# Optimization experiments

Measured on AMD Instinct MI355X. Metric: run time of the kernel, lower is better.

The kernel has to match this reference:

```python
import jax, jax.numpy as jnp
import numpy as np
from jax import lax

D_MODEL = 512
D_STATE = 32
D_CONV = 4
D_INNER = 2 * D_MODEL
DT_RANK = (D_MODEL + 15) // 16  # 32
B_SZ, L = 8, 1024
EPS = 1e-12


def _mamba_params(key, pfx):
    ks = jax.random.split(key, 6)
    s = 0.02
    p = {}
    p[pfx + '_in_w'] = jax.random.normal(ks[0], (2 * D_INNER, D_MODEL)) * s
    p[pfx + '_conv_w'] = jax.random.normal(ks[1], (D_INNER, D_CONV)) * s
    p[pfx + '_conv_b'] = jnp.zeros((D_INNER,))
    p[pfx + '_xproj_w'] = jax.random.normal(ks[2], (DT_RANK + 2 * D_STATE, D_INNER)) * s
    p[pfx + '_dt_w'] = jax.random.normal(ks[3], (D_INNER, DT_RANK)) * s
    p[pfx + '_dt_b'] = jax.random.uniform(ks[4], (D_INNER,), minval=-4.0, maxval=-2.0)
    p[pfx + '_A_log'] = jnp.log(jnp.broadcast_to(jnp.arange(1, D_STATE + 1, dtype=jnp.float32), (D_INNER, D_STATE)))
    p[pfx + '_D'] = jnp.ones((D_INNER,))
    p[pfx + '_out_w'] = jax.random.normal(ks[5], (D_MODEL, D_INNER)) * s
    return p


def setup_inputs() -> dict:
    key = jax.random.key(0)
    ks = jax.random.split(key, 10)
    inp = {
        'hidden_states': jax.random.normal(ks[0], (B_SZ, L, D_MODEL)),
        'lengths': jax.random.randint(ks[1], (B_SZ,), 1, L + 1, dtype=jnp.int32),
    }
    inp.update(_mamba_params(ks[2], 'f'))
    inp.update(_mamba_params(ks[3], 'b'))
    s = 0.02
    inp['proj_w'] = jax.random.normal(ks[4], (1, 2)) * 0.5 + 0.5
    inp['proj_b'] = jnp.zeros((1,))
    inp['ln_g'] = jnp.ones((D_MODEL,))
    inp['ln_b'] = jnp.zeros((D_MODEL,))
    inp['ffn_w1'] = jax.random.normal(ks[5], (4 * D_MODEL, D_MODEL)) * s
    inp['ffn_b1'] = jnp.zeros((4 * D_MODEL,))
    inp['ffn_w2'] = jax.random.normal(ks[6], (D_MODEL, 4 * D_MODEL)) * s
    inp['ffn_b2'] = jnp.zeros((D_MODEL,))
    inp['ffn_ln_g'] = jnp.ones((D_MODEL,))
    inp['ffn_ln_b'] = jnp.zeros((D_MODEL,))
    return inp


def _layernorm(x, g, b):
    mu = jnp.mean(x, -1, keepdims=True)
    var = jnp.mean(jnp.square(x - mu), -1, keepdims=True)
    return (x - mu) * lax.rsqrt(var + EPS) * g + b


def _selective_scan(delta, Bm, Cm, u, A, D):
    # delta,u: (B,L,Di); Bm,Cm: (B,L,N); A: (Di,N); D: (Di,)
    def step(h, inp):
        d_t, B_t, C_t, u_t = inp
        dA = jnp.exp(d_t[..., None] * A)                 # (B,Di,N)
        h = dA * h + (d_t * u_t)[..., None] * B_t[:, None, :]
        y = jnp.einsum('bdn,bn->bd', h, C_t)
        return h, y
    h0 = jnp.zeros((u.shape[0], A.shape[0], A.shape[1]), u.dtype)
    xs = (delta.transpose(1, 0, 2), Bm.transpose(1, 0, 2),
          Cm.transpose(1, 0, 2), u.transpose(1, 0, 2))
    _, ys = lax.scan(step, h0, xs)
    return ys.transpose(1, 0, 2) + u * D


def _mamba(x, in_w, conv_w, conv_b, xproj_w, dt_w, dt_b, A_log, Dp, out_w):
    xz = jnp.einsum('bld,ed->ble', x, in_w)              # (B,L,2Di)
    x_in, z = jnp.split(xz, 2, axis=-1)
    # causal depthwise conv1d
    xc = jnp.pad(x_in.transpose(0, 2, 1), ((0, 0), (0, 0), (D_CONV - 1, 0)))
    xc = lax.conv_general_dilated(xc, conv_w[:, None, :], (1,), 'VALID',
                                  dimension_numbers=('NCH', 'OIH', 'NCH'),
                                  feature_group_count=D_INNER)
    xc = jax.nn.silu(xc + conv_b[None, :, None]).transpose(0, 2, 1)  # (B,L,Di)
    x_dbl = jnp.einsum('bld,ed->ble', xc, xproj_w)
    dt, Bm, Cm = jnp.split(x_dbl, [DT_RANK, DT_RANK + D_STATE], axis=-1)
    delta = jax.nn.softplus(jnp.einsum('blr,dr->bld', dt, dt_w) + dt_b)
    A = -jnp.exp(A_log)
    y = _selective_scan(delta, Bm, Cm, xc, A, Dp)
    y = y * jax.nn.silu(z)
    return jnp.einsum('bld,ed->ble', y, out_w)


def reference(hidden_states, lengths,
              f_in_w, f_conv_w, f_conv_b, f_xproj_w, f_dt_w, f_dt_b, f_A_log, f_D, f_out_w,
              b_in_w, b_conv_w, b_conv_b, b_xproj_w, b_dt_w, b_dt_b, b_A_log, b_D, b_out_w,
              proj_w, proj_b, ln_g, ln_b,
              ffn_w1, ffn_b1, ffn_w2, ffn_b2, ffn_ln_g, ffn_ln_b):
    x = hidden_states
    hf = _mamba(x, f_in_w, f_conv_w, f_conv_b, f_xproj_w, f_dt_w, f_dt_b, f_A_log, f_D, f_out_w)
    hb = _mamba(jnp.flip(x, 1), b_in_w, b_conv_w, b_conv_b, b_xproj_w, b_dt_w, b_dt_b, b_A_log, b_D, b_out_w)
    hb = jnp.flip(hb, 1)
    # Linear(2,1) over stacked [hf,hb] on last axis
    out = hf * proj_w[0, 0] + hb * proj_w[0, 1] + proj_b[0]
    out1 = _layernorm(out + x, ln_g, ln_b)  # dropout = identity (eval)
    h = jax.nn.gelu(jnp.einsum('bld,ed->ble', out1, ffn_w1) + ffn_b1, approximate=False)
    h = jnp.einsum('ble,de->bld', h, ffn_w2) + ffn_b2
    return _layernorm(h + out1, ffn_ln_g, ffn_ln_b)
```

## Files before the change

### kernel.cpp

```cpp
#include <hip/hip_runtime.h>
#include <hip/hip_bf16.h>
#include <hip/hip_fp16.h>
#include <math.h>

typedef __hip_bfloat16 bf16;
typedef __attribute__((ext_vector_type(8))) short bfrag;
typedef __attribute__((ext_vector_type(4))) float ffrag;
typedef __attribute__((ext_vector_type(4))) float f4;
typedef __attribute__((ext_vector_type(4))) short sh4;

#define BSZ    8
#define LSEQ   1024
#define DMODEL 512
#define DINNER 1024
#define DSTATE 32
#define DTRANK 32
#define MROWS  (BSZ * LSEQ)

__device__ __forceinline__ float bf2f(bf16 v) { return __bfloat162float(v); }
__device__ __forceinline__ float s2f(short s) {
    union { unsigned u; float f; } c; c.u = ((unsigned)(unsigned short)s) << 16; return c.f;
}
__device__ __forceinline__ short f2s(float v) {
    union { bf16 b; short s; } u; u.b = __float2bfloat16(v); return u.s;
}
__device__ __forceinline__ void stC(float* p, size_t i, float v) { p[i] = v; }
__device__ __forceinline__ void stC(bf16* p, size_t i, float v) { p[i] = __float2bfloat16(v); }
__device__ __forceinline__ float fsigmoid(float x) {
    return __builtin_amdgcn_rcpf(1.f + __expf(-x));
}
__device__ __forceinline__ float fexp2(float x) { return __builtin_amdgcn_exp2f(x); }

__device__ __forceinline__ float dload(const void* p, size_t i, int f) {
    if (f == 1) return ((const float*)p)[i];
    if (f == 2) return __half2float(((const __half*)p)[i]);
    if (f == 3) return (float)((const double*)p)[i];
    return bf2f(((const bf16*)p)[i]);
}

enum { ACT_NONE = 0, ACT_SOFTPLUS = 1, ACT_GELU = 2 };

__global__ void resolve_kernel(const void* a8, const void* d9, const void* d22,
                               const void* s0, const void* s1, int* flags)
{
    if (blockIdx.x != 0) return;
    const int lane = threadIdx.x;
    const int cand[4] = {1, 0, 2, 3};
    int fw = -1;
    for (int ci = 0; ci < 4 && fw < 0; ++ci) {
        int f = cand[ci];
        bool ok = true;
        if (lane < 48) {
            float e = logf((float)((lane & 31) + 1));
            float v = dload(a8, lane, f);
            ok = (v == v) && fabsf(v - e) <= 0.02f * e + 0.02f;
        } else if (lane < 56) {
            int k = lane - 48;
            ok = fabsf(dload(d9, k, f) - 1.f) <= 0.01f &&
                 fabsf(dload(d22, k, f) - 1.f) <= 0.01f;
        }
        if (__all(ok)) fw = f;
    }
    int fx = -1, xs = -1;
    for (int si = 0; si < 2 && fx < 0; ++si) {
        const void* p = (si == 0) ? s0 : s1;
        for (int ci = 0; ci < 4 && fx < 0; ++ci) {
            int f = cand[ci];
            bool ok = true;
            float s = 0.f, s2 = 0.f;
            for (int k = lane; k < 256; k += 64) {
                float v = dload(p, k, f);
                ok = ok && (v == v) && fabsf(v) < 16.f;
                s += v; s2 += v * v;
            }
            int allok = __all(ok);
            for (int m = 1; m < 64; m <<= 1) {
                s += __shfl_xor(s, m); s2 += __shfl_xor(s2, m);
            }
            if (allok) {
                float mu = s * (1.f / 256.f);
                float var = s2 * (1.f / 256.f) - mu * mu;
                if (var > 0.25f && var < 4.f) { fx = f; xs = si; }
            }
        }
    }
    if (lane == 0) {
        flags[0] = (fw < 0) ? 1 : fw;
        flags[1] = (fx < 0) ? 1 : fx;
        flags[2] = (xs < 0) ? 0 : xs;
        flags[3] = (fw == 1 && fx == 1) ? 1 : 0;
    }
}

__global__ __launch_bounds__(256) void cvt_x_kernel(const void* x0, const void* x1,
                                                    bf16* __restrict__ dst,
                                                    const int* __restrict__ flags)
{
    const void* x = flags[2] ? x1 : x0;
    const int fx = flags[1];
    int i = blockIdx.x * 256 + threadIdx.x;
    if (fx == 1) {
        f4 v = ((const f4*)x)[i];
        sh4 o;
#pragma unroll
        for (int j = 0; j < 4; ++j) o[j] = f2s(v[j]);
        ((sh4*)dst)[i] = o;
    } else {
#pragma unroll
        for (int j = 0; j < 4; ++j)
            dst[(size_t)i * 4 + j] = __float2bfloat16(dload(x, (size_t)i * 4 + j, fx));
    }
}

__device__ __forceinline__ void cvt_one(const float* s, bf16* d, int off)
{
    f4 v = ((const f4*)s)[off];
    sh4 o;
#pragma unroll
    for (int j = 0; j < 4; ++j) o[j] = f2s(v[j]);
    ((sh4*)d)[off] = o;
}

__global__ __launch_bounds__(256) void cvt6_kernel(
    const float* s0, bf16* d0, int n0, const float* s1, bf16* d1, int n1,
    const float* s2, bf16* d2, int n2, const float* s3, bf16* d3, int n3,
    const float* s4, bf16* d4, int n4, const float* s5, bf16* d5, int n5)
{
    int i = blockIdx.x * 256 + threadIdx.x;
    if (i < n0) { cvt_one(s0, d0, i); return; } i -= n0;
    if (i < n1) { cvt_one(s1, d1, i); return; } i -= n1;
    if (i < n2) { cvt_one(s2, d2, i); return; } i -= n2;
    if (i < n3) { cvt_one(s3, d3, i); return; } i -= n3;
    if (i < n4) { cvt_one(s4, d4, i); return; } i -= n4;
    if (i < n5) cvt_one(s5, d5, i);
}

__global__ __launch_bounds__(256) void transpose_kernel(
    const bf16* __restrict__ src, bf16* __restrict__ dst, int R, int D)
{
    __shared__ short t[64][72];
    const int r0 = blockIdx.x * 64, d0 = blockIdx.y * 64;
    const int tr = threadIdx.x >> 3;
    const int tc = (threadIdx.x & 7) * 8;
#pragma unroll
    for (int h = 0; h < 2; ++h) {
        int d = tr + h * 32;
        bfrag v = *(const bfrag*)&src[(size_t)(d0 + d) * R + r0 + tc];
#pragma unroll
        for (int j = 0; j < 8; ++j) t[tc + j][d] = v[j];
    }
    __syncthreads();
#pragma unroll
    for (int h = 0; h < 2; ++h) {
        int r = tr + h * 32;
        bfrag v = *(const bfrag*)&t[r][tc];
        *(bfrag*)&dst[(size_t)(r0 + r) * D + d0 + tc] = v;
    }
}

__global__ __launch_bounds__(256) void conv8_kernel(
    const bf16* __restrict__ xin_T,
    const void* __restrict__ cw, const void* __restrict__ cb,
    bf16* __restrict__ u_T,
    const int* __restrict__ flags)
{
    const int fw = flags[0];
    int blk = blockIdx.x;
    int chunk = blk & 3;
    int d = blk >> 2;
    int m = chunk * 2048 + threadIdx.x * 8;
    size_t base = (size_t)d * MROWS;
    float w0 = dload(cw, d * 4 + 0, fw), w1 = dload(cw, d * 4 + 1, fw);
    float w2 = dload(cw, d * 4 + 2, fw), w3 = dload(cw, d * 4 + 3, fw);
    float cbv = dload(cb, d, fw);
    const bf16* src = &xin_T[base + m];
    bfrag v = *(const bfrag*)src;
    float x[11];
    if (m & (LSEQ - 1)) {
        bfrag pv = *(const bfrag*)(src - 8);
        x[0] = s2f(pv[5]); x[1] = s2f(pv[6]); x[2] = s2f(pv[7]);
    } else { x[0] = 0.f; x[1] = 0.f; x[2] = 0.f; }
#pragma unroll
    for (int j = 0; j < 8; ++j) x[3 + j] = s2f(v[j]);
    bfrag o;
#pragma unroll
    for (int j = 0; j < 8; ++j) {
        float a = cbv + x[j] * w0 + x[j + 1] * w1 + x[j + 2] * w2 + x[j + 3] * w3;
        a = a * fsigmoid(a);
        o[j] = f2s(a);
    }
    *(bfrag*)&u_T[base + m] = o;
}

__device__ __forceinline__ void glds16(const bf16* g, short* l)
{
    __builtin_amdgcn_global_load_lds(
        (const __attribute__((address_space(1))) void*)g,
        (__attribute__((address_space(3))) void*)l,
        16, 0, 0);
}

template <int FLIPB, int ACT, typename CT>
__global__ __launch_bounds__(256) void bgemm_kernel(
    const bf16* __restrict__ A, int lda,
    const bf16* __restrict__ B, int ldb,
    const float* __restrict__ bias,
    CT* __restrict__ C, int ldc, int K)
{
    __shared__ __align__(16) short As[2][128 * 32];
    __shared__ __align__(16) short Bs[2][128 * 32];
    const int tid = threadIdx.x;
    const int bm = blockIdx.y * 128, bn = blockIdx.x * 128;
    const int lane = tid & 63, w = tid >> 6;

    const int srow = lane >> 2;
    const int skc  = (lane & 3) << 3;
    const int arow0 = bm + w * 32 + srow;
    int brow0 = bn + w * 32 + srow;
    int brow1 = brow0 + 16;
    if (FLIPB) {
        brow0 = (brow0 & ~(LSEQ - 1)) + (LSEQ - 1 - (brow0 & (LSEQ - 1)));
        brow1 = (brow1 & ~(LSEQ - 1)) + (LSEQ - 1 - (brow1 & (LSEQ - 1)));
    }
    const bf16* ga0 = A + (size_t)arow0 * lda + skc;
    const bf16* ga1 = ga0 + (size_t)16 * lda;
    const bf16* gb0 = B + (size_t)brow0 * ldb + skc;
    const bf16* gb1 = B + (size_t)brow1 * ldb + skc;
    const int lA0 = (w * 32) * 32, lA1 = (w * 32 + 16) * 32;

    const int wm = (w & 1) << 6, wn = (w >> 1) << 6;
    const int lm = lane & 15, quad = lane >> 4;

    ffrag acc[4][4];
#pragma unroll
    for (int i = 0; i < 4; ++i)
#pragma unroll
        for (int j = 0; j < 4; ++j)
#pragma unroll
            for (int e = 0; e < 4; ++e) acc[i][j][e] = 0.f;

#define BG_STAGE(buf, kk)                      \
    do {                                       \
        glds16(ga0 + (kk), &As[buf][lA0]);     \
        glds16(ga1 + (kk), &As[buf][lA1]);     \
        glds16(gb0 + (kk), &Bs[buf][lA0]);     \
        glds16(gb1 + (kk), &Bs[buf][lA1]);     \
    } while (0)

#define BG_COMPUTE(buf)                                                        \
    do {                                                                       \
        bfrag af[4], bfv[4];                                                   \
        _Pragma("unroll")                                                      \
        for (int ti = 0; ti < 4; ++ti)                                         \
            af[ti] = *(const bfrag*)&As[buf][(wm + ti * 16 + lm) * 32 + quad * 8]; \
        _Pragma("unroll")                                                      \
        for (int tj = 0; tj < 4; ++tj)                                         \
            bfv[tj] = *(const bfrag*)&Bs[buf][(wn + tj * 16 + lm) * 32 + quad * 8]; \
        __builtin_amdgcn_s_setprio(1);                                         \
        _Pragma("unroll")                                                      \
        for (int ti = 0; ti < 4; ++ti)                                         \
            _Pragma("unroll")                                                  \
            for (int tj = 0; tj < 4; ++tj)                                     \
                acc[ti][tj] = __builtin_amdgcn_mfma_f32_16x16x32_bf16(         \
                    af[ti], bfv[tj], acc[ti][tj], 0, 0, 0);                    \
        __builtin_amdgcn_s_setprio(0);                                         \
    } while (0)

    BG_STAGE(0, 0);
    BG_STAGE(1, 32);
    int cur = 0;
    for (int k0 = 0; k0 < K - 32; k0 += 32) {
        asm volatile("s_waitcnt vmcnt(4)" ::: "memory");
        __builtin_amdgcn_s_barrier();
        __builtin_amdgcn_sched_barrier(0);
        BG_COMPUTE(cur);
        __builtin_amdgcn_s_barrier();
        __builtin_amdgcn_sched_barrier(0);
        if (k0 + 64 < K) BG_STAGE(cur, k0 + 64);
        cur ^= 1;
    }
    asm volatile("s_waitcnt vmcnt(0)" ::: "memory");
    __builtin_amdgcn_s_barrier();
    __builtin_amdgcn_sched_barrier(0);
    BG_COMPUTE(cur);
#undef BG_STAGE
#undef BG_COMPUTE

#pragma unroll
    for (int tj = 0; tj < 4; ++tj) {
        int col = bn + wn + tj * 16 + lm;
        float bcv = bias ? bias[col] : 0.f;
#pragma unroll
        for (int ti = 0; ti < 4; ++ti) {
#pragma unroll
            for (int r2 = 0; r2 < 4; ++r2) {
                int rowg = bm + wm + ti * 16 + quad * 4 + r2;
                float v = acc[ti][tj][r2] + bcv;
                if (ACT == ACT_GELU) v = 0.5f * v * (1.f + erff(v * 0.70710678118654752f));
                stC(C, (size_t)rowg * ldc + col, v);
            }
        }
    }
}

template <int ACT, int XPROJ, int RES, typename CT>
__global__ __launch_bounds__(256) void bgemm64_kernel(
    const bf16* __restrict__ A, int lda,
    const bf16* __restrict__ B, int ldb,
    const float* __restrict__ bias,
    CT* __restrict__ C, int ldc,
    float* __restrict__ C2,
    const bf16* __restrict__ res,
    int M, int K)
{
    __shared__ __align__(16) short As[2][128 * 64];
    __shared__ __align__(16) short Bs[2][64 * 64];
    const int tid = threadIdx.x;
    const int bm = blockIdx.y * 128, bn = blockIdx.x * 64;
    const int lane = tid & 63, w = tid >> 6;

    const int lr = lane >> 3;
    const int sc = ((lane & 7) ^ lr) << 3;

    const bf16* ga[4];
#pragma unroll
    for (int a = 0; a < 4; ++a) {
        int ar = bm + w * 32 + a * 8 + lr;
        if (ar >= M) ar = M - 1;
        ga[a] = A + (size_t)ar * lda + sc;
    }
    const bf16* gb[2];
#pragma unroll
    for (int a = 0; a < 2; ++a) {
        int br = bn + w * 16 + a * 8 + lr;
        gb[a] = B + (size_t)br * ldb + sc;
    }
    const int lA = (w * 32) * 64, lB = (w * 16) * 64;

    const int wm = (w & 1) << 6, wn = (w >> 1) << 5;
    const int lm = lane & 15, quad = lane >> 4;

    ffrag acc[4][2];
#pragma unroll
    for (int i = 0; i < 4; ++i)
#pragma unroll
        for (int j = 0; j < 2; ++j)
#pragma unroll
            for (int e = 0; e < 4; ++e) acc[i][j][e] = 0.f;

#define BG64_STAGE(buf, kk)                                              \
    do {                                                                 \
        _Pragma("unroll")                                                \
        for (int a = 0; a < 4; ++a)                                      \
            glds16(ga[a] + (kk), &As[buf][lA + a * 8 * 64]);             \
        _Pragma("unroll")                                                \
        for (int a = 0; a < 2; ++a)                                      \
            glds16(gb[a] + (kk), &Bs[buf][lB + a * 8 * 64]);             \
    } while (0)

#define BG64_COMPUTE(buf)                                                      \
    do {                                                                       \
        bfrag af[2][4], bfv[2][2];                                             \
        _Pragma("unroll")                                                      \
        for (int kk = 0; kk < 2; ++kk) {                                       \
            _Pragma("unroll")                                                  \
            for (int ti = 0; ti < 4; ++ti) {                                   \
                int row = wm + ti * 16 + lm;                                   \
                int c = kk * 4 + quad;                                         \
                af[kk][ti] = *(const bfrag*)&As[buf][row * 64 + ((c ^ (row & 7)) << 3)]; \
            }                                                                  \
            _Pragma("unroll")                                                  \
            for (int tj = 0; tj < 2; ++tj) {                                   \
                int row = wn + tj * 16 + lm;                                   \
                int c = kk * 4 + quad;                                         \
                bfv[kk][tj] = *(const bfrag*)&Bs[buf][row * 64 + ((c ^ (row & 7)) << 3)]; \
            }                                                                  \
        }                                                                      \
        __builtin_amdgcn_s_setprio(1);                                         \
        _Pragma("unroll")                                                      \
        for (int kk = 0; kk < 2; ++kk)                                         \
            _Pragma("unroll")                                                  \
            for (int ti = 0; ti < 4; ++ti)                                     \
                _Pragma("unroll")                                              \
                for (int tj = 0; tj < 2; ++tj)                                 \
                    acc[ti][tj] = __builtin_amdgcn_mfma_f32_16x16x32_bf16(     \
                        af[kk][ti], bfv[kk][tj], acc[ti][tj], 0, 0, 0);        \
        __builtin_amdgcn_s_setprio(0);                                         \
    } while (0)

    BG64_STAGE(0, 0);
    BG64_STAGE(1, 64);
    int cur = 0;
    for (int k0 = 0; k0 < K - 64; k0 += 64) {
        asm volatile("s_waitcnt vmcnt(6)" ::: "memory");
        __builtin_amdgcn_s_barrier();
        __builtin_amdgcn_sched_barrier(0);
        BG64_COMPUTE(cur);
        __builtin_amdgcn_s_barrier();
        __builtin_amdgcn_sched_barrier(0);
        if (k0 + 128 < K) BG64_STAGE(cur, k0 + 128);
        cur ^= 1;
    }
    asm volatile("s_waitcnt vmcnt(0)" ::: "memory");
    __builtin_amdgcn_s_barrier();
    __builtin_amdgcn_sched_barrier(0);
    BG64_COMPUTE(cur);
#undef BG64_STAGE
#undef BG64_COMPUTE

#pragma unroll
    for (int tj = 0; tj < 2; ++tj) {
        int col = bn + wn + tj * 16 + lm;
        float bcv = bias ? bias[col] : 0.f;
#pragma unroll
        for (int ti = 0; ti < 4; ++ti) {
#pragma unroll
            for (int r2 = 0; r2 < 4; ++r2) {
                int rowg = bm + wm + ti * 16 + quad * 4 + r2;
                if (XPROJ) {
                    float v = acc[ti][tj][r2];
                    if (rowg < 32)
                        ((float*)C)[(size_t)rowg * ldc + col] = v;
                    else if (rowg < 96)
                        C2[(((size_t)col >> 3) * 64 + (rowg - 32)) * 8 + (col & 7)] = v;
                } else if (rowg < M) {
                    float v = acc[ti][tj][r2] + bcv;
                    if (ACT == ACT_GELU) v = 0.5f * v * (1.f + erff(v * 0.70710678118654752f));
                    if (RES) v += bf2f(res[(size_t)rowg * ldc + col]);
                    stC(C, (size_t)rowg * ldc + col, v);
                }
            }
        }
    }
}

__global__ __launch_bounds__(256) void dt_kernel(
    const float* __restrict__ xdT,
    const float* __restrict__ dt_w,
    const float* __restrict__ dt_b,
    bf16* __restrict__ delta_T)
{
    const int m = blockIdx.x * 256 + threadIdx.x;
    const int d0 = blockIdx.y * 64;
    float v[32];
#pragma unroll
    for (int r = 0; r < 32; ++r) v[r] = xdT[(size_t)r * MROWS + m];
    for (int d = d0; d < d0 + 64; ++d) {
        float acc = dt_b[d];
#pragma unroll
        for (int r = 0; r < 32; ++r) acc = fmaf(dt_w[d * 32 + r], v[r], acc);
        acc = (acc > 20.f) ? acc : log1pf(__expf(acc));
        delta_T[(size_t)d * MROWS + m] = __float2bfloat16(acc);
    }
}

#define SCH 8
struct ScanBuf { float dl[SCH], uv[SCH], Bv[SCH], Cv[SCH]; float zsc, usc; };

__device__ __forceinline__ void scan_load(ScanBuf& s,
    const bf16* __restrict__ dT, const bf16* __restrict__ uT,
    const bf16* __restrict__ zT, const float* __restrict__ xm,
    size_t lb, int coff, int n)
{
    bfrag dv = *(const bfrag*)&dT[lb];
    bfrag uv = *(const bfrag*)&uT[lb];
#pragma unroll
    for (int j = 0; j < SCH; ++j) { s.dl[j] = s2f(dv[j]); s.uv[j] = s2f(uv[j]); }
    s.zsc = bf2f(zT[lb + (n & 7)]);
    s.usc = bf2f(uT[lb + (n & 7)]);
    const float* bp = xm + coff + n * 8;
    f4 b0 = *(const f4*)bp;
    f4 b1 = *(const f4*)(bp + 4);
    const float* cp = bp + 256;
    f4 c0 = *(const f4*)cp;
    f4 c1 = *(const f4*)(cp + 4);
#pragma unroll
    for (int j = 0; j < 4; ++j) {
        s.Bv[j] = b0[j]; s.Bv[4 + j] = b1[j];
        s.Cv[j] = c0[j]; s.Cv[4 + j] = c1[j];
    }
}

__device__ __forceinline__ void scan_compute(const ScanBuf& s, float& h,
    float Ad2, float Dd, bf16* __restrict__ yT, size_t lb,
    bool b0, bool b1, bool b2, bool wr)
{
    float p[SCH];
#pragma unroll
    for (int j = 0; j < SCH; ++j) {
        float dlv = s.dl[j];
        h = fexp2(dlv * Ad2) * h + dlv * s.uv[j] * s.Bv[j];
        p[j] = h * s.Cv[j];
    }
    float q[4];
#pragma unroll
    for (int jj = 0; jj < 4; ++jj) {
        float keep = b0 ? p[2 * jj + 1] : p[2 * jj];
        float send = b0 ? p[2 * jj] : p[2 * jj + 1];
        q[jj] = keep + __shfl_xor(send, 1);
    }
    float r0 = (b1 ? q[1] : q[0]) + __shfl_xor(b1 ? q[0] : q[1], 2);
    float r1 = (b1 ? q[3] : q[2]) + __shfl_xor(b1 ? q[2] : q[3], 2);
    float t = (b2 ? r1 : r0) + __shfl_xor(b2 ? r0 : r1, 4);
    t += __shfl_xor(t, 8);
    t += __shfl_xor(t, 16);
    if (wr) {
        float y = t + s.usc * Dd;
        float g = s.zsc;
        y *= g * fsigmoid(g);
        yT[lb + (threadIdx.x & 7)] = __float2bfloat16(y);
    }
}

__global__ __launch_bounds__(256) void scan_kernel(
    const bf16* __restrict__ delta_T,
    bf16* __restrict__ u_T,
    const bf16* __restrict__ z_T,
    const float* __restrict__ xdbl_m,
    const void* __restrict__ A_log,
    const void* __restrict__ Dp,
    const int* __restrict__ flags)
{
    const int fw = flags[0];
    const int tid = threadIdx.x;
    const int n = tid & 31;
    const int dloc = tid >> 5;
    const int gd = blockIdx.x * 8 + dloc;
    const int b = gd >> 10;
    const int d = gd & (DINNER - 1);
    const bool b0 = n & 1, b1 = n & 2, b2 = n & 4;
    const bool wr = (n < 8);

    const float Ad2 = -__expf(dload(A_log, d * DSTATE + n, fw)) * 1.44269504088896341f;
    const float Dd = dload(Dp, d, fw);
    const size_t lbase = (size_t)d * MROWS + b * LSEQ;
    const float* xmb = xdbl_m + ((size_t)b * LSEQ >> 3) * 512;
    float h = 0.f;

    ScanBuf bufA, bufB;
    scan_load(bufA, delta_T, u_T, z_T, xmb, lbase, 0, n);
    for (int c0 = 0; c0 < LSEQ / SCH; c0 += 2) {
        scan_load(bufB, delta_T, u_T, z_T, xmb,
                  lbase + (size_t)(c0 + 1) * SCH, (c0 + 1) * 512, n);
        scan_compute(bufA, h, Ad2, Dd, u_T, lbase + (size_t)c0 * SCH, b0, b1, b2, wr);
        if (c0 + 2 < LSEQ / SCH)
            scan_load(bufA, delta_T, u_T, z_T, xmb,
                      lbase + (size_t)(c0 + 2) * SCH, (c0 + 2) * 512, n);
        scan_compute(bufB, h, Ad2, Dd, u_T, lbase + (size_t)(c0 + 1) * SCH, b0, b1, b2, wr);
    }
}

__global__ __launch_bounds__(256) void combine_cvt_kernel(
    const bf16* __restrict__ hf, const bf16* __restrict__ hb,
    const void* __restrict__ x0, const void* __restrict__ x1,
    const void* __restrict__ pw, const void* __restrict__ pb,
    const void* __restrict__ g, const void* __restrict__ be,
    bf16* __restrict__ out1,
    const float* __restrict__ w1s, bf16* __restrict__ w1d,
    const float* __restrict__ w2s, bf16* __restrict__ w2d,
    const int* __restrict__ flags)
{
    if (blockIdx.x >= 2048) {
        int i = (blockIdx.x - 2048) * 256 + threadIdx.x;
        const int nw = (2048 * 512) / 4;
        if (i < nw) cvt_one(w1s, w1d, i);
        else cvt_one(w2s, w2d, i - nw);
        return;
    }
    const int fw = flags[0];
    const int fx = flags[1];
    const void* x = flags[2] ? x1 : x0;
    const int lane = threadIdx.x & 63;
    int row = blockIdx.x * 4 + (threadIdx.x >> 6);
    int b = row >> 10, l = row & (LSEQ - 1);
    int rrow = (b << 10) + (LSEQ - 1 - l);
    float pw0 = dload(pw, 0, fw), pw1 = dload(pw, 1, fw), pbv = dload(pb, 0, fw);
    int c0 = lane * 8;
    bfrag hfv = *(const bfrag*)&hf[(size_t)row * DMODEL + c0];
    bfrag hbv = *(const bfrag*)&hb[(size_t)rrow * DMODEL + c0];
    float v[8], s = 0.f, s2 = 0.f;
#pragma unroll
    for (int j = 0; j < 8; ++j) {
        float val = s2f(hfv[j]) * pw0 + s2f(hbv[j]) * pw1 + pbv
                  + dload(x, (size_t)row * DMODEL + c0 + j, fx);
        v[j] = val; s += val; s2 += val * val;
    }
#pragma unroll
    for (int m = 1; m < 64; m <<= 1) { s += __shfl_xor(s, m); s2 += __shfl_xor(s2, m); }
    float mu = s * (1.f / DMODEL);
    float var = s2 * (1.f / DMODEL) - mu * mu;
    float r = rsqrtf(fmaxf(var, 0.f) + 1e-12f);
    bfrag o;
#pragma unroll
    for (int j = 0; j < 8; ++j)
        o[j] = f2s((v[j] - mu) * r * dload(g, c0 + j, fw) + dload(be, c0 + j, fw));
    *(bfrag*)&out1[(size_t)row * DMODEL + c0] = o;
}

__global__ __launch_bounds__(256) void final_ln_kernel(
    const float* __restrict__ out2,
    const void* __restrict__ g, const void* __restrict__ be,
    float* __restrict__ out,
    const int* __restrict__ flags)
{
    const int fw = flags[0];
    const int valid = flags[3];
    const int lane = threadIdx.x & 63;
    int row = blockIdx.x * 4 + (threadIdx.x >> 6);
    int c0 = lane * 8;
    f4 a0 = *(const f4*)&out2[(size_t)row * DMODEL + c0];
    f4 a1 = *(const f4*)&out2[(size_t)row * DMODEL + c0 + 4];
    float v[8], s = 0.f, s2 = 0.f;
#pragma unroll
    for (int j = 0; j < 4; ++j) { v[j] = a0[j]; v[4 + j] = a1[j]; }
#pragma unroll
    for (int j = 0; j < 8; ++j) { s += v[j]; s2 += v[j] * v[j]; }
#pragma unroll
    for (int m = 1; m < 64; m <<= 1) { s += __shfl_xor(s, m); s2 += __shfl_xor(s2, m); }
    float mu = s * (1.f / DMODEL);
    float var = s2 * (1.f / DMODEL) - mu * mu;
    float r = rsqrtf(fmaxf(var, 0.f) + 1e-12f);
    f4 o0, o1;
#pragma unroll
    for (int j = 0; j < 8; ++j) {
        float val = (v[j] - mu) * r * dload(g, c0 + j, fw) + dload(be, c0 + j, fw);
        val = valid ? val : 0.f;
        if (j < 4) o0[j] = val; else o1[j - 4] = val;
    }
    *(f4*)&out[(size_t)row * DMODEL + c0] = o0;
    *(f4*)&out[(size_t)row * DMODEL + c0 + 4] = o1;
}

extern "C" void kernel_launch(void* const* d_in, const int* in_sizes, int n_in,
                              void* d_out, int out_size, void* d_ws, size_t ws_size,
                              hipStream_t stream)
{
    const void* x0 = d_in[0];
    const void* x1 = d_in[1];
    const void* proj_w   = d_in[20];
    const void* proj_b   = d_in[21];
    const void* ln_g     = d_in[22];
    const void* ln_b     = d_in[23];
    const float* ffn_w1  = (const float*)d_in[24];
    const float* ffn_b1  = (const float*)d_in[25];
    const float* ffn_w2  = (const float*)d_in[26];
    const float* ffn_b2  = (const float*)d_in[27];
    const void* ffn_ln_g = d_in[28];
    const void* ffn_ln_b = d_in[29];

    char* wsb = (char*)d_ws;
    char* ob  = (char*)d_out;
    bf16*  xin_T   = (bf16*)(wsb + 0);
    bf16*  z_T     = (bf16*)(wsb + (16u << 20));
    bf16*  uy_T    = (bf16*)(wsb + (32u << 20));
    bf16*  u_rm    = (bf16*)(wsb + 0);
    bf16*  delta_T = (bf16*)(wsb + 0);
    bf16*  y_rm    = (bf16*)(wsb + 0);
    float* xdT     = (float*)(wsb + (48u << 20));
    bf16*  in_w_bf0 = (bf16*)(wsb + (49u << 20));
    float* xdbl_m   = (float*)(wsb + (49u << 20));
    bf16*  in_w_bf1 = (bf16*)(wsb + (51u << 20));
    bf16*  xp_w_bf0 = (bf16*)(wsb + (53u << 20));
    bf16*  xp_w_bf1 = (bf16*)(wsb + (53u << 20) + (256u << 10));
    bf16*  o_w_bf0  = (bf16*)(wsb + (54u << 20));
    bf16*  o_w_bf1  = (bf16*)(wsb + (55u << 20));
    bf16*  hf      = (bf16*)d_out;
    bf16*  hb      = (bf16*)d_out + (size_t)MROWS * DMODEL;
    bf16*  xbf     = (bf16*)(ob + (8u << 20));
    bf16*  w1bf    = (bf16*)(ob + 0);
    bf16*  w2bf    = (bf16*)(ob + (2u << 20));
    bf16*  out1    = (bf16*)(wsb + 0);
    bf16*  ffn_h   = (bf16*)(wsb + (8u << 20));
    float* out2    = (float*)(wsb + (40u << 20));
    int*   flags   = (int*)(wsb + (56u << 20));

    dim3 blk(256);

    resolve_kernel<<<dim3(1), dim3(64), 0, stream>>>(
        d_in[8], d_in[9], d_in[22], x0, x1, flags);
    cvt_x_kernel<<<dim3(4096), blk, 0, stream>>>(x0, x1, xbf, flags);
    cvt6_kernel<<<dim3(3264), blk, 0, stream>>>(
        (const float*)d_in[2],  in_w_bf0, (2048 * 512) / 4,
        (const float*)d_in[11], in_w_bf1, (2048 * 512) / 4,
        (const float*)d_in[5],  xp_w_bf0, (96 * 1024) / 4,
        (const float*)d_in[14], xp_w_bf1, (96 * 1024) / 4,
        (const float*)d_in[10], o_w_bf0,  (512 * 1024) / 4,
        (const float*)d_in[19], o_w_bf1,  (512 * 1024) / 4);

    for (int dir = 0; dir < 2; ++dir) {
        int pb0 = 2 + dir * 9;
        const void*  conv_w  = d_in[pb0 + 1];
        const void*  conv_b  = d_in[pb0 + 2];
        const float* dt_w    = (const float*)d_in[pb0 + 4];
        const float* dt_b    = (const float*)d_in[pb0 + 5];
        const void*  A_log   = d_in[pb0 + 6];
        const void*  Dp      = d_in[pb0 + 7];
        bf16* in_w_bf = dir ? in_w_bf1 : in_w_bf0;
        bf16* xp_w_bf = dir ? xp_w_bf1 : xp_w_bf0;
        bf16* o_w_bf  = dir ? o_w_bf1  : o_w_bf0;
        bf16* hout = (dir == 0) ? hf : hb;

        if (dir == 0)
            bgemm_kernel<0, ACT_NONE, bf16><<<dim3(64, 16), blk, 0, stream>>>(
                in_w_bf, DMODEL, xbf, DMODEL, nullptr, xin_T, MROWS, DMODEL);
        else
            bgemm_kernel<1, ACT_NONE, bf16><<<dim3(64, 16), blk, 0, stream>>>(
                in_w_bf, DMODEL, xbf, DMODEL, nullptr, xin_T, MROWS, DMODEL);

        conv8_kernel<<<dim3(DINNER * 4), blk, 0, stream>>>(
            xin_T, conv_w, conv_b, uy_T, flags);
        transpose_kernel<<<dim3(128, 16), blk, 0, stream>>>(uy_T, u_rm, MROWS, DINNER);
        bgemm64_kernel<ACT_NONE, 1, 0, float><<<dim3(128, 1), blk, 0, stream>>>(
            xp_w_bf, DINNER, u_rm, DINNER, nullptr,
            xdT, MROWS, xdbl_m, nullptr, 96, DINNER);
        dt_kernel<<<dim3(32, 16), blk, 0, stream>>>(xdT, dt_w, dt_b, delta_T);
        scan_kernel<<<dim3((BSZ * DINNER) / 8), blk, 0, stream>>>(
            delta_T, uy_T, z_T, xdbl_m, A_log, Dp, flags);
        transpose_kernel<<<dim3(128, 16), blk, 0, stream>>>(uy_T, y_rm, MROWS, DINNER);
        bgemm64_kernel<ACT_NONE, 0, 0, bf16><<<dim3(8, 64), blk, 0, stream>>>(
            y_rm, DINNER, o_w_bf, DINNER, nullptr, hout, DMODEL, nullptr, nullptr,
            MROWS, DINNER);
    }

    combine_cvt_kernel<<<dim3(4096), blk, 0, stream>>>(
        hf, hb, x0, x1, proj_w, proj_b, ln_g, ln_b, out1,
        ffn_w1, w1bf, ffn_w2, w2bf, flags);
    bgemm_kernel<0, ACT_GELU, bf16><<<dim3(16, 64), blk, 0, stream>>>(
        out1, DMODEL, w1bf, DMODEL, ffn_b1, ffn_h, 2048, DMODEL);
    bgemm64_kernel<ACT_NONE, 0, 1, float><<<dim3(8, 64), blk, 0, stream>>>(
        ffn_h, 2048, w2bf, 2048, ffn_b2, out2, DMODEL, nullptr, out1,
        MROWS, 2048);
    final_ln_kernel<<<dim3(MROWS / 4), blk, 0, stream>>>(
        out2, ffn_ln_g, ffn_ln_b, (float*)d_out, flags);
}
```

Baseline: 807.4 us.

## Triple-buffer GEMM LDS pipeline and fuse dtype resolve into weight conversion

The bf16 GEMM goes from a double-buffered to a triple-buffered LDS pipeline that prefetches two K-steps ahead, with vmcnt waits graded by how many stages remain. The goal is to hide more global-load latency behind MFMA work. The cost is 50% more shared memory per block, which may lower occupancy. Separately, the one-block dtype-resolve kernel is merged into the weight-conversion kernel as an extra block, removing one launch.

```diff
diff --git a/kernel.cpp b/kernel.cpp
--- a/kernel.cpp
+++ b/kernel.cpp
@@ -40,56 +40,79 @@
 
 enum { ACT_NONE = 0, ACT_SOFTPLUS = 1, ACT_GELU = 2 };
 
-__global__ void resolve_kernel(const void* a8, const void* d9, const void* d22,
-                               const void* s0, const void* s1, int* flags)
-{
-    if (blockIdx.x != 0) return;
-    const int lane = threadIdx.x;
-    const int cand[4] = {1, 0, 2, 3};
-    int fw = -1;
-    for (int ci = 0; ci < 4 && fw < 0; ++ci) {
-        int f = cand[ci];
-        bool ok = true;
-        if (lane < 48) {
-            float e = logf((float)((lane & 31) + 1));
-            float v = dload(a8, lane, f);
-            ok = (v == v) && fabsf(v - e) <= 0.02f * e + 0.02f;
-        } else if (lane < 56) {
-            int k = lane - 48;
-            ok = fabsf(dload(d9, k, f) - 1.f) <= 0.01f &&
-                 fabsf(dload(d22, k, f) - 1.f) <= 0.01f;
-        }
-        if (__all(ok)) fw = f;
-    }
-    int fx = -1, xs = -1;
-    for (int si = 0; si < 2 && fx < 0; ++si) {
-        const void* p = (si == 0) ? s0 : s1;
-        for (int ci = 0; ci < 4 && fx < 0; ++ci) {
+__device__ __forceinline__ void cvt_one(const float* s, bf16* d, int off)
+{
+    f4 v = ((const f4*)s)[off];
+    sh4 o;
+#pragma unroll
+    for (int j = 0; j < 4; ++j) o[j] = f2s(v[j]);
+    ((sh4*)d)[off] = o;
+}
+
+__global__ __launch_bounds__(256) void resolve_cvt6_kernel(
+    const void* a8, const void* d9, const void* d22,
+    const void* s0v, const void* s1v, int* flags,
+    const float* s0, bf16* d0, int n0, const float* s1, bf16* d1, int n1,
+    const float* s2, bf16* d2, int n2, const float* s3, bf16* d3, int n3,
+    const float* s4, bf16* d4, int n4, const float* s5, bf16* d5, int n5)
+{
+    if (blockIdx.x == 0) {
+        if (threadIdx.x >= 64) return;
+        const int lane = threadIdx.x;
+        const int cand[4] = {1, 0, 2, 3};
+        int fw = -1;
+        for (int ci = 0; ci < 4 && fw < 0; ++ci) {
             int f = cand[ci];
             bool ok = true;
-            float s = 0.f, s2 = 0.f;
-            for (int k = lane; k < 256; k += 64) {
-                float v = dload(p, k, f);
-                ok = ok && (v == v) && fabsf(v) < 16.f;
-                s += v; s2 += v * v;
+            if (lane < 48) {
+                float e = logf((float)((lane & 31) + 1));
+                float v = dload(a8, lane, f);
+                ok = (v == v) && fabsf(v - e) <= 0.02f * e + 0.02f;
+            } else if (lane < 56) {
+                int k = lane - 48;
+                ok = fabsf(dload(d9, k, f) - 1.f) <= 0.01f &&
+                     fabsf(dload(d22, k, f) - 1.f) <= 0.01f;
             }
-            int allok = __all(ok);
-            for (int m = 1; m < 64; m <<= 1) {
-                s += __shfl_xor(s, m); s2 += __shfl_xor(s2, m);
-            }
-            if (allok) {
-                float mu = s * (1.f / 256.f);
-                float var = s2 * (1.f / 256.f) - mu * mu;
-                if (var > 0.25f && var < 4.f) { fx = f; xs = si; }
+            if (__all(ok)) fw = f;
+        }
+        int fx = -1, xs = -1;
+        for (int si = 0; si < 2 && fx < 0; ++si) {
+            const void* p = (si == 0) ? s0v : s1v;
+            for (int ci = 0; ci < 4 && fx < 0; ++ci) {
+                int f = cand[ci];
+                bool ok = true;
+                float s = 0.f, s2a = 0.f;
+                for (int k = lane; k < 256; k += 64) {
+                    float v = dload(p, k, f);
+                    ok = ok && (v == v) && fabsf(v) < 16.f;
+                    s += v; s2a += v * v;
+                }
+                int allok = __all(ok);
+                for (int m = 1; m < 64; m <<= 1) {
+                    s += __shfl_xor(s, m); s2a += __shfl_xor(s2a, m);
+                }
+                if (allok) {
+                    float mu = s * (1.f / 256.f);
+                    float var = s2a * (1.f / 256.f) - mu * mu;
+                    if (var > 0.25f && var < 4.f) { fx = f; xs = si; }
+                }
             }
         }
-    }
-    if (lane == 0) {
-        flags[0] = (fw < 0) ? 1 : fw;
-        flags[1] = (fx < 0) ? 1 : fx;
-        flags[2] = (xs < 0) ? 0 : xs;
-        flags[3] = (fw == 1 && fx == 1) ? 1 : 0;
-    }
+        if (lane == 0) {
+            flags[0] = (fw < 0) ? 1 : fw;
+            flags[1] = (fx < 0) ? 1 : fx;
+            flags[2] = (xs < 0) ? 0 : xs;
+            flags[3] = (fw == 1 && fx == 1) ? 1 : 0;
+        }
+        return;
+    }
+    int i = (blockIdx.x - 1) * 256 + threadIdx.x;
+    if (i < n0) { cvt_one(s0, d0, i); return; } i -= n0;
+    if (i < n1) { cvt_one(s1, d1, i); return; } i -= n1;
+    if (i < n2) { cvt_one(s2, d2, i); return; } i -= n2;
+    if (i < n3) { cvt_one(s3, d3, i); return; } i -= n3;
+    if (i < n4) { cvt_one(s4, d4, i); return; } i -= n4;
+    if (i < n5) cvt_one(s5, d5, i);
 }
 
 __global__ __launch_bounds__(256) void cvt_x_kernel(const void* x0, const void* x1,
@@ -110,29 +133,6 @@
         for (int j = 0; j < 4; ++j)
             dst[(size_t)i * 4 + j] = __float2bfloat16(dload(x, (size_t)i * 4 + j, fx));
     }
-}
-
-__device__ __forceinline__ void cvt_one(const float* s, bf16* d, int off)
-{
-    f4 v = ((const f4*)s)[off];
-    sh4 o;
-#pragma unroll
-    for (int j = 0; j < 4; ++j) o[j] = f2s(v[j]);
-    ((sh4*)d)[off] = o;
-}
-
-__global__ __launch_bounds__(256) void cvt6_kernel(
-    const float* s0, bf16* d0, int n0, const float* s1, bf16* d1, int n1,
-    const float* s2, bf16* d2, int n2, const float* s3, bf16* d3, int n3,
-    const float* s4, bf16* d4, int n4, const float* s5, bf16* d5, int n5)
-{
-    int i = blockIdx.x * 256 + threadIdx.x;
-    if (i < n0) { cvt_one(s0, d0, i); return; } i -= n0;
-    if (i < n1) { cvt_one(s1, d1, i); return; } i -= n1;
-    if (i < n2) { cvt_one(s2, d2, i); return; } i -= n2;
-    if (i < n3) { cvt_one(s3, d3, i); return; } i -= n3;
-    if (i < n4) { cvt_one(s4, d4, i); return; } i -= n4;
-    if (i < n5) cvt_one(s5, d5, i);
 }
 
 __global__ __launch_bounds__(256) void transpose_kernel(
@@ -207,8 +207,8 @@
     const float* __restrict__ bias,
     CT* __restrict__ C, int ldc, int K)
 {
-    __shared__ __align__(16) short As[2][128 * 32];
-    __shared__ __align__(16) short Bs[2][128 * 32];
+    __shared__ __align__(16) short As[3][128 * 32];
+    __shared__ __align__(16) short Bs[3][128 * 32];
     const int tid = threadIdx.x;
     const int bm = blockIdx.y * 128, bn = blockIdx.x * 128;
     const int lane = tid & 63, w = tid >> 6;
@@ -268,21 +268,22 @@
 
     BG_STAGE(0, 0);
     BG_STAGE(1, 32);
-    int cur = 0;
-    for (int k0 = 0; k0 < K - 32; k0 += 32) {
-        asm volatile("s_waitcnt vmcnt(4)" ::: "memory");
+    BG_STAGE(2, 64);
+    const int nIter = K >> 5;
+    int buf = 0;
+    for (int i = 0; i < nIter; ++i) {
+        int rem = nIter - 1 - i;
+        if (rem >= 2)      asm volatile("s_waitcnt vmcnt(8)" ::: "memory");
+        else if (rem == 1) asm volatile("s_waitcnt vmcnt(4)" ::: "memory");
+        else               asm volatile("s_waitcnt vmcnt(0)" ::: "memory");
         __builtin_amdgcn_s_barrier();
         __builtin_amdgcn_sched_barrier(0);
-        BG_COMPUTE(cur);
+        BG_COMPUTE(buf);
         __builtin_amdgcn_s_barrier();
         __builtin_amdgcn_sched_barrier(0);
-        if (k0 + 64 < K) BG_STAGE(cur, k0 + 64);
-        cur ^= 1;
-    }
-    asm volatile("s_waitcnt vmcnt(0)" ::: "memory");
-    __builtin_amdgcn_s_barrier();
-    __builtin_amdgcn_sched_barrier(0);
-    BG_COMPUTE(cur);
+        if (i + 3 < nIter) BG_STAGE(buf, (i + 3) << 5);
+        buf = (buf == 2) ? 0 : buf + 1;
+    }
 #undef BG_STAGE
 #undef BG_COMPUTE
 
@@ -676,16 +677,15 @@
 
     dim3 blk(256);
 
-    resolve_kernel<<<dim3(1), dim3(64), 0, stream>>>(
-        d_in[8], d_in[9], d_in[22], x0, x1, flags);
-    cvt_x_kernel<<<dim3(4096), blk, 0, stream>>>(x0, x1, xbf, flags);
-    cvt6_kernel<<<dim3(3264), blk, 0, stream>>>(
+    resolve_cvt6_kernel<<<dim3(3265), blk, 0, stream>>>(
+        d_in[8], d_in[9], d_in[22], x0, x1, flags,
         (const float*)d_in[2],  in_w_bf0, (2048 * 512) / 4,
         (const float*)d_in[11], in_w_bf1, (2048 * 512) / 4,
         (const float*)d_in[5],  xp_w_bf0, (96 * 1024) / 4,
         (const float*)d_in[14], xp_w_bf1, (96 * 1024) / 4,
         (const float*)d_in[10], o_w_bf0,  (512 * 1024) / 4,
         (const float*)d_in[19], o_w_bf1,  (512 * 1024) / 4);
+    cvt_x_kernel<<<dim3(4096), blk, 0, stream>>>(x0, x1, xbf, flags);
 
     for (int dir = 0; dir < 2; ++dir) {
         int pb0 = 2 + dir * 9;
```

Result: no change. 820.3 us (+1.6%).
